# Performance work log

Hardware: AMD Instinct MI355X
Metric: run time of the kernel (lower is better)

## Reference

```python
import jax, jax.numpy as jnp
import numpy as np

BN_EPS = 1e-5

def _square_distance(src, dst):
    # src [B,N,3], dst [B,S,3] -> [B,N,S]
    d = -2.0 * jnp.einsum('bnc,bsc->bns', src, dst)
    d = d + jnp.sum(src * src, -1)[:, :, None]
    d = d + jnp.sum(dst * dst, -1)[:, None, :]
    return d

def _conv_bn_relu(x, w, b, g, beta):
    # x [B,C,N]; 1x1 conv == channel GEMM, then training-mode batchnorm over (B,N)
    y = jnp.einsum('oc,bcn->bon', w, x) + b[None, :, None]
    mean = jnp.mean(y, axis=(0, 2), keepdims=True)
    var = jnp.mean((y - mean) ** 2, axis=(0, 2), keepdims=True)  # biased, as torch BN uses for normalization
    y = (y - mean) * jax.lax.rsqrt(var + BN_EPS)
    y = y * g[None, :, None] + beta[None, :, None]
    return jax.nn.relu(y)

def setup_inputs() -> dict:
    key = jax.random.key(0)
    ks = jax.random.split(key, 8)
    B, N, S, D1, D2 = 8, 8192, 2048, 128, 256
    C_in, C_mid, C_out = D1 + D2, 256, 256
    return {
        'xyz1': jax.random.normal(ks[0], (B, 3, N), jnp.float32),
        'xyz2': jax.random.normal(ks[1], (B, 3, S), jnp.float32),
        'points1': jax.random.normal(ks[2], (B, D1, N), jnp.float32),
        'points2': jax.random.normal(ks[3], (B, D2, S), jnp.float32),
        'w1': jax.random.normal(ks[4], (C_mid, C_in), jnp.float32) * (1.0 / np.sqrt(C_in)),
        'b1': jax.random.normal(ks[5], (C_mid,), jnp.float32) * 0.01,
        'g1': jnp.ones((C_mid,), jnp.float32),
        'beta1': jnp.zeros((C_mid,), jnp.float32),
        'w2': jax.random.normal(ks[6], (C_out, C_mid), jnp.float32) * (1.0 / np.sqrt(C_mid)),
        'b2': jax.random.normal(ks[7], (C_out,), jnp.float32) * 0.01,
        'g2': jnp.ones((C_out,), jnp.float32),
        'beta2': jnp.zeros((C_out,), jnp.float32),
    }

def reference(xyz1, xyz2, points1, points2, w1, b1, g1, beta1, w2, b2, g2, beta2):
    B = xyz1.shape[0]
    p1xyz = jnp.transpose(xyz1, (0, 2, 1))      # [B,N,3]
    p2xyz = jnp.transpose(xyz2, (0, 2, 1))      # [B,S,3]
    p2 = jnp.transpose(points2, (0, 2, 1))      # [B,S,D2]

    dists = _square_distance(p1xyz, p2xyz)      # [B,N,S]
    neg_d3, idx = jax.lax.top_k(-dists, 3)      # 3 smallest distances
    d3 = -neg_d3                                # [B,N,3]
    recip = 1.0 / (d3 + 1e-8)
    weight = recip / jnp.sum(recip, axis=2, keepdims=True)  # [B,N,3]

    gathered = jax.vmap(lambda p, i: p[i])(p2, idx)          # [B,N,3,D2]
    interp = jnp.sum(gathered * weight[..., None], axis=2)   # [B,N,D2]

    new_points = jnp.concatenate([jnp.transpose(points1, (0, 2, 1)), interp], axis=-1)
    x = jnp.transpose(new_points, (0, 2, 1))    # [B,D1+D2,N]
    x = _conv_bn_relu(x, w1, b1, g1, beta1)
    x = _conv_bn_relu(x, w2, b2, g2, beta2)
    return x
```

## Files before the change

kernel.cpp:

```cpp
#include <hip/hip_runtime.h>

#define B_    8
#define N_    8192
#define S_    2048
#define D1_   128
#define D2_   256
#define CIN_  384
#define CMID_ 256
#define COUT_ 256

typedef unsigned int  u32;
typedef unsigned short u16;
typedef __attribute__((ext_vector_type(8))) short short8;
typedef __attribute__((ext_vector_type(4))) float f32x4;

static __device__ __forceinline__ u32 uminu(u32 a, u32 b) { return a < b ? a : b; }
static __device__ __forceinline__ u32 umaxu(u32 a, u32 b) { return a > b ? a : b; }
static __device__ __forceinline__ u32 umed3(u32 a, u32 b, u32 c) {
  u32 d;
  asm("v_med3_u32 %0, %1, %2, %3" : "=v"(d) : "v"(a), "v"(b), "v"(c));
  return d;
}
static __device__ __forceinline__ u16 f2bf(float f) {
  union { float f; u32 u; } v; v.f = f;
  u32 r = v.u + 0x7FFFu + ((v.u >> 16) & 1u);
  return (u16)(r >> 16);
}
static __device__ __forceinline__ float bflo(u32 u) { return __uint_as_float(u << 16); }
static __device__ __forceinline__ float bfhi(u32 u) { return __uint_as_float(u & 0xFFFF0000u); }

#define GLD16(g, l)                                                             \
  __builtin_amdgcn_global_load_lds((const __attribute__((address_space(1))) void*)(g), \
                                   (__attribute__((address_space(3))) void*)(l), 16, 0, 0)

__global__ __launch_bounds__(256) void k_prep(const float* __restrict__ xyz2,
                                              float4* __restrict__ pts4) {
  const int b = blockIdx.y, s = blockIdx.x * 256 + threadIdx.x;
  const float* xb = xyz2 + (size_t)b * 3 * S_;
  float x = xb[s], y = xb[S_ + s], z = xb[2 * S_ + s];
  pts4[b * S_ + s] = make_float4(-2.f * x, -2.f * y, -2.f * z, x * x + y * y + z * z);
}

__global__ __launch_bounds__(256) void k_nn_scan(const float* __restrict__ xyz1,
                                                 const float4* __restrict__ pts4,
                                                 uint4* __restrict__ keys) {
  const int b = blockIdx.z, chunk = blockIdx.y;
  const int n = blockIdx.x * 256 + threadIdx.x;
  const float* pb = xyz1 + (size_t)b * 3 * N_;
  const float px = pb[n], py = pb[N_ + n], pz = pb[2 * N_ + n];
  const float pn = px * px + py * py + pz * pz;
  const float4* __restrict__ P = pts4 + b * S_ + chunk * 256;
  u32 m0 = ~0u, m1 = ~0u, m2 = ~0u, m3 = ~0u;
#pragma unroll 8
  for (int s = 0; s < 256; ++s) {
    float4 q = P[s];
    float d = fmaf(px, q.x, fmaf(py, q.y, fmaf(pz, q.z, pn + q.w)));
    d = fmaxf(d, 0.f);
    u32 k = (__float_as_uint(d) & 0xFFFFFF00u) | (u32)s;
    m3 = uminu(m3, umaxu(m2, k));
    m2 = umed3(m1, m2, k);
    m1 = umed3(m0, m1, k);
    m0 = uminu(m0, k);
  }
  uint4 v; v.x = m0; v.y = m1; v.z = m2; v.w = m3;
  keys[((size_t)(b * 8 + chunk)) * N_ + n] = v;
}

__global__ __launch_bounds__(256) void k_refine(const float* __restrict__ xyz1,
                                                const float4* __restrict__ pts4,
                                                const uint4* __restrict__ keys,
                                                int4* __restrict__ idx4,
                                                float4* __restrict__ w4) {
  const int b = blockIdx.y, n = blockIdx.x * 256 + threadIdx.x;
  const float* pb = xyz1 + (size_t)b * 3 * N_;
  const double px = (double)pb[n], py = (double)pb[N_ + n], pz = (double)pb[2 * N_ + n];
  const double pn = px * px + py * py + pz * pz;
  double bd0 = 1e300, bd1 = 1e300, bd2 = 1e300;
  int bi0 = 1 << 30, bi1 = 1 << 30, bi2 = 1 << 30;
#pragma unroll
  for (int c = 0; c < 8; ++c) {
    uint4 kk = keys[((size_t)(b * 8 + c)) * N_ + n];
    u32 arr[4] = {kk.x, kk.y, kk.z, kk.w};
#pragma unroll
    for (int j = 0; j < 4; ++j) {
      int s = c * 256 + (int)(arr[j] & 255u);
      float4 q = pts4[b * S_ + s];
      double x = (double)(q.x * -0.5f), y = (double)(q.y * -0.5f), z = (double)(q.z * -0.5f);
      double dot = px * x + py * y + pz * z;
      double d = -2.0 * dot + (pn + (x * x + y * y + z * z));
      if (d < bd2 || (d == bd2 && s < bi2)) {
        if (d < bd1 || (d == bd1 && s < bi1)) {
          bd2 = bd1; bi2 = bi1;
          if (d < bd0 || (d == bd0 && s < bi0)) { bd1 = bd0; bi1 = bi0; bd0 = d; bi0 = s; }
          else                                  { bd1 = d;  bi1 = s; }
        } else { bd2 = d; bi2 = s; }
      }
    }
  }
  float f0 = (float)bd0, f1 = (float)bd1, f2 = (float)bd2;
  float r0 = 1.f / (f0 + 1e-8f), r1 = 1.f / (f1 + 1e-8f), r2 = 1.f / (f2 + 1e-8f);
  float rs = r0 + r1 + r2;
  w4[(size_t)b * N_ + n]   = make_float4(r0 / rs, r1 / rs, r2 / rs, 0.f);
  idx4[(size_t)b * N_ + n] = make_int4(bi0, bi1, bi2, 0);
}

__global__ __launch_bounds__(256) void k_p2t(const float* __restrict__ p2,
                                             float* __restrict__ p2T) {
  __shared__ float t[32][33];
  const int b = blockIdx.z, s0 = blockIdx.x * 32, d0 = blockIdx.y * 32;
  const int cc = threadIdx.x & 31, rr = threadIdx.x >> 5;
#pragma unroll
  for (int i = 0; i < 4; ++i) {
    int r = rr + i * 8;
    t[r][cc] = p2[((size_t)b * D2_ + d0 + r) * S_ + s0 + cc];
  }
  __syncthreads();
#pragma unroll
  for (int i = 0; i < 4; ++i) {
    int r = rr + i * 8;
    p2T[((size_t)b * S_ + s0 + r) * D2_ + d0 + cc] = t[cc][r];
  }
}

__global__ __launch_bounds__(256) void k_packp1(const float* __restrict__ p1,
                                                u16* __restrict__ xT) {
  __shared__ float t[32][33];
  const int b = blockIdx.z, n0 = blockIdx.x * 32, c0 = blockIdx.y * 32;
  const int cc = threadIdx.x & 31, rr = threadIdx.x >> 5;
#pragma unroll
  for (int i = 0; i < 4; ++i) {
    int r = rr + i * 8;
    t[r][cc] = p1[((size_t)b * D1_ + c0 + r) * N_ + n0 + cc];
  }
  __syncthreads();
#pragma unroll
  for (int i = 0; i < 4; ++i) {
    int r = rr + i * 8;
    xT[((size_t)b * N_ + n0 + r) * CIN_ + c0 + cc] = f2bf(t[cc][r]);
  }
}

__global__ __launch_bounds__(256) void k_gather_pack(const float* __restrict__ p2T,
                                                     const int4* __restrict__ idx4,
                                                     const float4* __restrict__ w4,
                                                     u16* __restrict__ xT) {
  const int b = blockIdx.y;
  const int wv = threadIdx.x >> 6, lane = threadIdx.x & 63;
  const int nbase = blockIdx.x * 16 + wv * 4;
  int4   id[4];
  float4 w[4];
#pragma unroll
  for (int i = 0; i < 4; ++i) {
    id[i] = idx4[(size_t)b * N_ + nbase + i];
    w[i]  = w4[(size_t)b * N_ + nbase + i];
  }
#pragma unroll
  for (int i = 0; i < 4; ++i) {
    const int n = nbase + i;
    const float4* r0 = (const float4*)(p2T + ((size_t)b * S_ + id[i].x) * D2_) + lane;
    const float4* r1 = (const float4*)(p2T + ((size_t)b * S_ + id[i].y) * D2_) + lane;
    const float4* r2 = (const float4*)(p2T + ((size_t)b * S_ + id[i].z) * D2_) + lane;
    float4 a = *r0, bb = *r1, cq = *r2;
    ushort4 pk;
    pk.x = f2bf(a.x * w[i].x + bb.x * w[i].y + cq.x * w[i].z);
    pk.y = f2bf(a.y * w[i].x + bb.y * w[i].y + cq.y * w[i].z);
    pk.z = f2bf(a.z * w[i].x + bb.z * w[i].y + cq.z * w[i].z);
    pk.w = f2bf(a.w * w[i].x + bb.w * w[i].y + cq.w * w[i].z);
    *(ushort4*)(xT + ((size_t)b * N_ + n) * CIN_ + D1_ + lane * 4) = pk;
  }
}

__global__ __launch_bounds__(256) void k_wcvt(const float* __restrict__ w1,
                                              const float* __restrict__ w2,
                                              u16* __restrict__ w1b,
                                              u16* __restrict__ w2b) {
  int i = blockIdx.x * 256 + threadIdx.x;
  if (i < CMID_ * CIN_) w1b[i] = f2bf(w1[i]);
  int j = i - CMID_ * CIN_;
  if (j >= 0 && j < COUT_ * CMID_) w2b[j] = f2bf(w2[j]);
}

__global__ __launch_bounds__(256) void k_gemm1(const u16* __restrict__ Wb,
                                               const float* __restrict__ bias,
                                               const u16* __restrict__ xT,
                                               u16* __restrict__ y1T,
                                               float* __restrict__ sum,
                                               float* __restrict__ sumsq) {
  __shared__ u16 As[2][4096];
  __shared__ u16 Bs[2][4096];
  __shared__ float s_sum[128], s_ssq[128];
  const int b = blockIdx.z, bm0 = blockIdx.y * 128, bn0 = blockIdx.x * 128;
  const int tid = threadIdx.x, w = tid >> 6, l = tid & 63;
  const int wm = w & 1, wn = w >> 1;
  const int lr = l >> 2, lc = l & 3;
  const int fm = l & 15, fq = l >> 4;
  const int clog = (lc ^ ((lr >> 1) & 3)) * 8;
  const int swz8 = (fq ^ ((fm >> 1) & 3)) * 8;
  if (tid < 128) { s_sum[tid] = 0.f; s_ssq[tid] = 0.f; }
  f32x4 acc[4][4];
#pragma unroll
  for (int i = 0; i < 4; ++i)
#pragma unroll
    for (int j = 0; j < 4; ++j) acc[i][j] = (f32x4){0.f, 0.f, 0.f, 0.f};

  const int NK = CIN_ / 32;
#pragma unroll
  for (int j = 0; j < 2; ++j) {
    int seg = w * 2 + j, row = seg * 16 + lr;
    GLD16(Wb + (size_t)(bm0 + row) * CIN_ + clog, &As[0][seg * 512]);
    GLD16(xT + ((size_t)b * N_ + bn0 + row) * CIN_ + clog, &Bs[0][seg * 512]);
  }
  for (int kk = 0; kk < NK; ++kk) {
    __syncthreads();
    const int cur = kk & 1;
    if (kk + 1 < NK) {
      const int k0 = (kk + 1) * 32, nxt = cur ^ 1;
#pragma unroll
      for (int j = 0; j < 2; ++j) {
        int seg = w * 2 + j, row = seg * 16 + lr;
        GLD16(Wb + (size_t)(bm0 + row) * CIN_ + k0 + clog, &As[nxt][seg * 512]);
        GLD16(xT + ((size_t)b * N_ + bn0 + row) * CIN_ + k0 + clog, &Bs[nxt][seg * 512]);
      }
    }
    short8 af[4], bfr[4];
#pragma unroll
    for (int f = 0; f < 4; ++f) {
      af[f]  = *(const short8*)&As[cur][(wm * 64 + f * 16 + fm) * 32 + swz8];
      bfr[f] = *(const short8*)&Bs[cur][(wn * 64 + f * 16 + fm) * 32 + swz8];
    }
#pragma unroll
    for (int i = 0; i < 4; ++i)
#pragma unroll
      for (int j = 0; j < 4; ++j)
        acc[i][j] = __builtin_amdgcn_mfma_f32_16x16x32_bf16(af[i], bfr[j], acc[i][j], 0, 0, 0);
  }
#pragma unroll
  for (int i = 0; i < 4; ++i) {
    int ob = bm0 + wm * 64 + i * 16 + fq * 4;
    float4 b4 = *(const float4*)(bias + ob);
    float sv0 = 0, sv1 = 0, sv2 = 0, sv3 = 0, qv0 = 0, qv1 = 0, qv2 = 0, qv3 = 0;
#pragma unroll
    for (int j = 0; j < 4; ++j) {
      int n = bn0 + wn * 64 + j * 16 + fm;
      ushort4 pk;
      pk.x = f2bf(acc[i][j][0] + b4.x);
      pk.y = f2bf(acc[i][j][1] + b4.y);
      pk.z = f2bf(acc[i][j][2] + b4.z);
      pk.w = f2bf(acc[i][j][3] + b4.w);
      *(ushort4*)(y1T + ((size_t)b * N_ + n) * CMID_ + ob) = pk;
      float v0 = bflo(pk.x), v1 = bflo(pk.y), v2 = bflo(pk.z), v3 = bflo(pk.w);
      sv0 += v0; sv1 += v1; sv2 += v2; sv3 += v3;
      qv0 = fmaf(v0, v0, qv0); qv1 = fmaf(v1, v1, qv1);
      qv2 = fmaf(v2, v2, qv2); qv3 = fmaf(v3, v3, qv3);
    }
#pragma unroll
    for (int m = 1; m <= 8; m <<= 1) {
      sv0 += __shfl_xor(sv0, m); sv1 += __shfl_xor(sv1, m);
      sv2 += __shfl_xor(sv2, m); sv3 += __shfl_xor(sv3, m);
      qv0 += __shfl_xor(qv0, m); qv1 += __shfl_xor(qv1, m);
      qv2 += __shfl_xor(qv2, m); qv3 += __shfl_xor(qv3, m);
    }
    if (fm == 0) {
      int ol = wm * 64 + i * 16 + fq * 4;
      atomicAdd(&s_sum[ol + 0], sv0); atomicAdd(&s_sum[ol + 1], sv1);
      atomicAdd(&s_sum[ol + 2], sv2); atomicAdd(&s_sum[ol + 3], sv3);
      atomicAdd(&s_ssq[ol + 0], qv0); atomicAdd(&s_ssq[ol + 1], qv1);
      atomicAdd(&s_ssq[ol + 2], qv2); atomicAdd(&s_ssq[ol + 3], qv3);
    }
  }
  __syncthreads();
  if (tid < 128) {
    atomicAdd(&sum[bm0 + tid], s_sum[tid]);
    atomicAdd(&sumsq[bm0 + tid], s_ssq[tid]);
  }
}

__global__ __launch_bounds__(256) void k_affine(const float* __restrict__ sum,
                                                const float* __restrict__ sumsq,
                                                const float* __restrict__ g,
                                                const float* __restrict__ beta,
                                                float* __restrict__ scale,
                                                float* __restrict__ shift) {
  int o = threadIdx.x;
  const float inv = 1.0f / (float)(B_ * N_);
  float m = sum[o] * inv;
  float var = sumsq[o] * inv - m * m;
  float sc = g[o] / sqrtf(var + 1e-5f);
  scale[o] = sc;
  shift[o] = beta[o] - m * sc;
}

__global__ __launch_bounds__(256) void k_gemm2(const u16* __restrict__ Wb2,
                                               const float* __restrict__ b2,
                                               const u16* __restrict__ y1T,
                                               const float* __restrict__ scale,
                                               const float* __restrict__ shift,
                                               u16* __restrict__ y2T,
                                               float* __restrict__ sum,
                                               float* __restrict__ sumsq) {
  __shared__ u16 As[2][4096];
  __shared__ u16 Bs[2][4096];
  __shared__ float s_sum[128], s_ssq[128];
  const int b = blockIdx.z, bm0 = blockIdx.y * 128, bn0 = blockIdx.x * 128;
  const int tid = threadIdx.x, w = tid >> 6, l = tid & 63;
  const int wm = w & 1, wn = w >> 1;
  const int lr = l >> 2, lc = l & 3;
  const int fm = l & 15, fq = l >> 4;
  const int clog = (lc ^ ((lr >> 1) & 3)) * 8;
  const int swz8 = (fq ^ ((fm >> 1) & 3)) * 8;
  const int bn_0 = tid >> 2, bcp0 = tid & 3;
  const int bn_1 = (tid + 256) >> 2, bcp1 = (tid + 256) & 3;
  const int bph0 = (bcp0 ^ ((bn_0 >> 1) & 3)) * 8;
  const int bph1 = (bcp1 ^ ((bn_1 >> 1) & 3)) * 8;
  if (tid < 128) { s_sum[tid] = 0.f; s_ssq[tid] = 0.f; }
  f32x4 acc[4][4];
#pragma unroll
  for (int i = 0; i < 4; ++i)
#pragma unroll
    for (int j = 0; j < 4; ++j) acc[i][j] = (f32x4){0.f, 0.f, 0.f, 0.f};

  const int NK = CMID_ / 32;

  auto bn_pack = [&](uint4 r, int c) -> uint4 {
    float4 sA = *(const float4*)(scale + c);
    float4 sB = *(const float4*)(scale + c + 4);
    float4 hA = *(const float4*)(shift + c);
    float4 hB = *(const float4*)(shift + c + 4);
    float v0 = fmaxf(fmaf(bflo(r.x), sA.x, hA.x), 0.f);
    float v1 = fmaxf(fmaf(bfhi(r.x), sA.y, hA.y), 0.f);
    float v2 = fmaxf(fmaf(bflo(r.y), sA.z, hA.z), 0.f);
    float v3 = fmaxf(fmaf(bfhi(r.y), sA.w, hA.w), 0.f);
    float v4 = fmaxf(fmaf(bflo(r.z), sB.x, hB.x), 0.f);
    float v5 = fmaxf(fmaf(bfhi(r.z), sB.y, hB.y), 0.f);
    float v6 = fmaxf(fmaf(bflo(r.w), sB.z, hB.z), 0.f);
    float v7 = fmaxf(fmaf(bfhi(r.w), sB.w, hB.w), 0.f);
    uint4 pk;
    pk.x = (u32)f2bf(v0) | ((u32)f2bf(v1) << 16);
    pk.y = (u32)f2bf(v2) | ((u32)f2bf(v3) << 16);
    pk.z = (u32)f2bf(v4) | ((u32)f2bf(v5) << 16);
    pk.w = (u32)f2bf(v6) | ((u32)f2bf(v7) << 16);
    return pk;
  };

  {
#pragma unroll
    for (int j = 0; j < 2; ++j) {
      int seg = w * 2 + j, row = seg * 16 + lr;
      GLD16(Wb2 + (size_t)(bm0 + row) * CMID_ + clog, &As[0][seg * 512]);
    }
    uint4 r0 = *(const uint4*)(y1T + ((size_t)b * N_ + bn0 + bn_0) * CMID_ + bcp0 * 8);
    uint4 r1 = *(const uint4*)(y1T + ((size_t)b * N_ + bn0 + bn_1) * CMID_ + bcp1 * 8);
    *(uint4*)&Bs[0][bn_0 * 32 + bph0] = bn_pack(r0, bcp0 * 8);
    *(uint4*)&Bs[0][bn_1 * 32 + bph1] = bn_pack(r1, bcp1 * 8);
  }
  for (int kk = 0; kk < NK; ++kk) {
    __syncthreads();
    const int cur = kk & 1;
    uint4 r0, r1;
    const bool have = (kk + 1 < NK);
    const int k0n = (kk + 1) * 32, nxt = cur ^ 1;
    if (have) {
      r0 = *(const uint4*)(y1T + ((size_t)b * N_ + bn0 + bn_0) * CMID_ + k0n + bcp0 * 8);
      r1 = *(const uint4*)(y1T + ((size_t)b * N_ + bn0 + bn_1) * CMID_ + k0n + bcp1 * 8);
#pragma unroll
      for (int j = 0; j < 2; ++j) {
        int seg = w * 2 + j, row = seg * 16 + lr;
        GLD16(Wb2 + (size_t)(bm0 + row) * CMID_ + k0n + clog, &As[nxt][seg * 512]);
      }
    }
    short8 af[4], bfr[4];
#pragma unroll
    for (int f = 0; f < 4; ++f) {
      af[f]  = *(const short8*)&As[cur][(wm * 64 + f * 16 + fm) * 32 + swz8];
      bfr[f] = *(const short8*)&Bs[cur][(wn * 64 + f * 16 + fm) * 32 + swz8];
    }
#pragma unroll
    for (int i = 0; i < 4; ++i)
#pragma unroll
      for (int j = 0; j < 4; ++j)
        acc[i][j] = __builtin_amdgcn_mfma_f32_16x16x32_bf16(af[i], bfr[j], acc[i][j], 0, 0, 0);
    if (have) {
      *(uint4*)&Bs[nxt][bn_0 * 32 + bph0] = bn_pack(r0, k0n + bcp0 * 8);
      *(uint4*)&Bs[nxt][bn_1 * 32 + bph1] = bn_pack(r1, k0n + bcp1 * 8);
    }
  }
#pragma unroll
  for (int i = 0; i < 4; ++i) {
    int ob = bm0 + wm * 64 + i * 16 + fq * 4;
    float4 b4 = *(const float4*)(b2 + ob);
    float sv0 = 0, sv1 = 0, sv2 = 0, sv3 = 0, qv0 = 0, qv1 = 0, qv2 = 0, qv3 = 0;
#pragma unroll
    for (int j = 0; j < 4; ++j) {
      int n = bn0 + wn * 64 + j * 16 + fm;
      ushort4 pk;
      pk.x = f2bf(acc[i][j][0] + b4.x);
      pk.y = f2bf(acc[i][j][1] + b4.y);
      pk.z = f2bf(acc[i][j][2] + b4.z);
      pk.w = f2bf(acc[i][j][3] + b4.w);
      *(ushort4*)(y2T + ((size_t)b * N_ + n) * COUT_ + ob) = pk;
      float v0 = bflo(pk.x), v1 = bflo(pk.y), v2 = bflo(pk.z), v3 = bflo(pk.w);
      sv0 += v0; sv1 += v1; sv2 += v2; sv3 += v3;
      qv0 = fmaf(v0, v0, qv0); qv1 = fmaf(v1, v1, qv1);
      qv2 = fmaf(v2, v2, qv2); qv3 = fmaf(v3, v3, qv3);
    }
#pragma unroll
    for (int m = 1; m <= 8; m <<= 1) {
      sv0 += __shfl_xor(sv0, m); sv1 += __shfl_xor(sv1, m);
      sv2 += __shfl_xor(sv2, m); sv3 += __shfl_xor(sv3, m);
      qv0 += __shfl_xor(qv0, m); qv1 += __shfl_xor(qv1, m);
      qv2 += __shfl_xor(qv2, m); qv3 += __shfl_xor(qv3, m);
    }
    if (fm == 0) {
      int ol = wm * 64 + i * 16 + fq * 4;
      atomicAdd(&s_sum[ol + 0], sv0); atomicAdd(&s_sum[ol + 1], sv1);
      atomicAdd(&s_sum[ol + 2], sv2); atomicAdd(&s_sum[ol + 3], sv3);
      atomicAdd(&s_ssq[ol + 0], qv0); atomicAdd(&s_ssq[ol + 1], qv1);
      atomicAdd(&s_ssq[ol + 2], qv2); atomicAdd(&s_ssq[ol + 3], qv3);
    }
  }
  __syncthreads();
  if (tid < 128) {
    atomicAdd(&sum[bm0 + tid], s_sum[tid]);
    atomicAdd(&sumsq[bm0 + tid], s_ssq[tid]);
  }
}

__global__ __launch_bounds__(256) void k_bn2t(const u16* __restrict__ y2T,
                                              const float* __restrict__ scale,
                                              const float* __restrict__ shift,
                                              float* __restrict__ out) {
  __shared__ float t[32][33];
  const int b = blockIdx.z, n0 = blockIdx.x * 32, o0 = blockIdx.y * 32;
  const int cc = threadIdx.x & 31, rr = threadIdx.x >> 5;
  const float sc = scale[o0 + cc], sh = shift[o0 + cc];
#pragma unroll
  for (int i = 0; i < 4; ++i) {
    int r = rr + i * 8;
    float v = bflo((u32)y2T[((size_t)b * N_ + n0 + r) * COUT_ + o0 + cc]);
    t[r][cc] = fmaxf(fmaf(v, sc, sh), 0.f);
  }
  __syncthreads();
#pragma unroll
  for (int i = 0; i < 4; ++i) {
    int r = rr + i * 8;
    out[((size_t)b * COUT_ + o0 + r) * N_ + n0 + cc] = t[cc][r];
  }
}

extern "C" void kernel_launch(void* const* d_in, const int* in_sizes, int n_in,
                              void* d_out, int out_size, void* d_ws, size_t ws_size,
                              hipStream_t stream) {
  const float* xyz1    = (const float*)d_in[0];
  const float* xyz2    = (const float*)d_in[1];
  const float* points1 = (const float*)d_in[2];
  const float* points2 = (const float*)d_in[3];
  const float* w1      = (const float*)d_in[4];
  const float* b1      = (const float*)d_in[5];
  const float* g1      = (const float*)d_in[6];
  const float* beta1   = (const float*)d_in[7];
  const float* w2      = (const float*)d_in[8];
  const float* b2      = (const float*)d_in[9];
  const float* g2      = (const float*)d_in[10];
  const float* beta2   = (const float*)d_in[11];
  float* out = (float*)d_out;

  char* ws = (char*)d_ws;
  size_t off = 0;
  u16*    xT    = (u16*)(ws + off);    off += (size_t)B_ * N_ * CIN_ * 2;
  u16*    y1T   = (u16*)(ws + off);    off += (size_t)B_ * N_ * CMID_ * 2;
  float*  p2T   = (float*)(ws + off);  off += (size_t)B_ * S_ * D2_ * 4;
  float4* pts4  = (float4*)(ws + off); off += (size_t)B_ * S_ * 16;
  uint4*  keys  = (uint4*)(ws + off);  off += (size_t)B_ * 8 * N_ * 16;
  int4*   idx4  = (int4*)(ws + off);   off += (size_t)B_ * N_ * 16;
  float4* w4    = (float4*)(ws + off); off += (size_t)B_ * N_ * 16;
  u16*    w1b   = (u16*)(ws + off);    off += (size_t)CMID_ * CIN_ * 2;
  u16*    w2b   = (u16*)(ws + off);    off += (size_t)COUT_ * CMID_ * 2;
  float*  stats = (float*)(ws + off);
  u16*    y2T   = xT;

  hipMemsetAsync(stats, 0, 1024 * sizeof(float), stream);

  k_wcvt       <<<dim3((CMID_ * CIN_ + COUT_ * CMID_) / 256), 256, 0, stream>>>(w1, w2, w1b, w2b);
  k_prep       <<<dim3(S_ / 256, B_), 256, 0, stream>>>(xyz2, pts4);
  k_p2t        <<<dim3(S_ / 32, D2_ / 32, B_), 256, 0, stream>>>(points2, p2T);
  k_nn_scan    <<<dim3(N_ / 256, 8, B_), 256, 0, stream>>>(xyz1, pts4, keys);
  k_refine     <<<dim3(N_ / 256, B_), 256, 0, stream>>>(xyz1, pts4, keys, idx4, w4);
  k_packp1     <<<dim3(N_ / 32, D1_ / 32, B_), 256, 0, stream>>>(points1, xT);
  k_gather_pack<<<dim3(N_ / 16, B_), 256, 0, stream>>>(p2T, idx4, w4, xT);
  k_gemm1      <<<dim3(N_ / 128, CMID_ / 128, B_), 256, 0, stream>>>(w1b, b1, xT, y1T,
                                                                     stats + 0, stats + 256);
  k_affine     <<<1, 256, 0, stream>>>(stats + 0, stats + 256, g1, beta1, stats + 1024, stats + 1280);
  k_gemm2      <<<dim3(N_ / 128, COUT_ / 128, B_), 256, 0, stream>>>(w2b, b2, y1T,
                                                                     stats + 1024, stats + 1280,
                                                                     y2T, stats + 512, stats + 768);
  k_affine     <<<1, 256, 0, stream>>>(stats + 512, stats + 768, g2, beta2, stats + 1536, stats + 1792);
  k_bn2t       <<<dim3(N_ / 32, COUT_ / 32, B_), 256, 0, stream>>>(y2T, stats + 1536, stats + 1792, out);
}
```

Measured before the change: 297.7 us.

## Load GEMM fragments directly from global into registers, drop LDS staging

```diff
diff --git a/kernel.cpp b/kernel.cpp
--- a/kernel.cpp
+++ b/kernel.cpp
@@ -28,10 +28,11 @@
 }
 static __device__ __forceinline__ float bflo(u32 u) { return __uint_as_float(u << 16); }
 static __device__ __forceinline__ float bfhi(u32 u) { return __uint_as_float(u & 0xFFFF0000u); }
-
-#define GLD16(g, l)                                                             \
-  __builtin_amdgcn_global_load_lds((const __attribute__((address_space(1))) void*)(g), \
-                                   (__attribute__((address_space(3))) void*)(l), 16, 0, 0)
+static __device__ __forceinline__ u32 cvtpk_bf16(float lo, float hi) {
+  u32 d;
+  asm("v_cvt_pk_bf16_f32 %0, %1, %2" : "=v"(d) : "v"(lo), "v"(hi));
+  return d;
+}
 
 __global__ __launch_bounds__(256) void k_prep(const float* __restrict__ xyz2,
                                               float4* __restrict__ pts4) {
@@ -180,60 +181,59 @@
   if (j >= 0 && j < COUT_ * CMID_) w2b[j] = f2bf(w2[j]);
 }
 
+#define MFMA16(AF, BF)                                                          \
+  {                                                                             \
+    _Pragma("unroll") for (int i_ = 0; i_ < 4; ++i_) {                          \
+      _Pragma("unroll") for (int j_ = 0; j_ < 4; ++j_) {                        \
+        acc[i_][j_] = __builtin_amdgcn_mfma_f32_16x16x32_bf16(                  \
+            AF[i_], BF[j_], acc[i_][j_], 0, 0, 0);                              \
+      }                                                                         \
+    }                                                                           \
+  }
+
 __global__ __launch_bounds__(256) void k_gemm1(const u16* __restrict__ Wb,
                                                const float* __restrict__ bias,
                                                const u16* __restrict__ xT,
                                                u16* __restrict__ y1T,
                                                float* __restrict__ sum,
                                                float* __restrict__ sumsq) {
-  __shared__ u16 As[2][4096];
-  __shared__ u16 Bs[2][4096];
   __shared__ float s_sum[128], s_ssq[128];
   const int b = blockIdx.z, bm0 = blockIdx.y * 128, bn0 = blockIdx.x * 128;
   const int tid = threadIdx.x, w = tid >> 6, l = tid & 63;
   const int wm = w & 1, wn = w >> 1;
-  const int lr = l >> 2, lc = l & 3;
   const int fm = l & 15, fq = l >> 4;
-  const int clog = (lc ^ ((lr >> 1) & 3)) * 8;
-  const int swz8 = (fq ^ ((fm >> 1) & 3)) * 8;
   if (tid < 128) { s_sum[tid] = 0.f; s_ssq[tid] = 0.f; }
+
+  const u16* Ab = Wb + (size_t)(bm0 + wm * 64 + fm) * CIN_ + fq * 8;
+  const u16* Bb = xT + ((size_t)b * N_ + bn0 + wn * 64 + fm) * CIN_ + fq * 8;
+
   f32x4 acc[4][4];
 #pragma unroll
   for (int i = 0; i < 4; ++i)
 #pragma unroll
     for (int j = 0; j < 4; ++j) acc[i][j] = (f32x4){0.f, 0.f, 0.f, 0.f};
 
+#define LDA_G1(dst, kk)                                                         \
+  { _Pragma("unroll") for (int i_ = 0; i_ < 4; ++i_)                            \
+      dst[i_] = *(const short8*)(Ab + (size_t)i_ * 16 * CIN_ + (kk) * 32); }
+#define LDB_G1(dst, kk)                                                         \
+  { _Pragma("unroll") for (int i_ = 0; i_ < 4; ++i_)                            \
+      dst[i_] = *(const short8*)(Bb + (size_t)i_ * 16 * CIN_ + (kk) * 32); }
+
   const int NK = CIN_ / 32;
-#pragma unroll
-  for (int j = 0; j < 2; ++j) {
-    int seg = w * 2 + j, row = seg * 16 + lr;
-    GLD16(Wb + (size_t)(bm0 + row) * CIN_ + clog, &As[0][seg * 512]);
-    GLD16(xT + ((size_t)b * N_ + bn0 + row) * CIN_ + clog, &Bs[0][seg * 512]);
-  }
-  for (int kk = 0; kk < NK; ++kk) {
-    __syncthreads();
-    const int cur = kk & 1;
-    if (kk + 1 < NK) {
-      const int k0 = (kk + 1) * 32, nxt = cur ^ 1;
-#pragma unroll
-      for (int j = 0; j < 2; ++j) {
-        int seg = w * 2 + j, row = seg * 16 + lr;
-        GLD16(Wb + (size_t)(bm0 + row) * CIN_ + k0 + clog, &As[nxt][seg * 512]);
-        GLD16(xT + ((size_t)b * N_ + bn0 + row) * CIN_ + k0 + clog, &Bs[nxt][seg * 512]);
-      }
-    }
-    short8 af[4], bfr[4];
-#pragma unroll
-    for (int f = 0; f < 4; ++f) {
-      af[f]  = *(const short8*)&As[cur][(wm * 64 + f * 16 + fm) * 32 + swz8];
-      bfr[f] = *(const short8*)&Bs[cur][(wn * 64 + f * 16 + fm) * 32 + swz8];
-    }
-#pragma unroll
-    for (int i = 0; i < 4; ++i)
-#pragma unroll
-      for (int j = 0; j < 4; ++j)
-        acc[i][j] = __builtin_amdgcn_mfma_f32_16x16x32_bf16(af[i], bfr[j], acc[i][j], 0, 0, 0);
-  }
+  short8 A0[4], B0[4], A1[4], B1[4];
+  LDA_G1(A0, 0); LDB_G1(B0, 0);
+#pragma unroll
+  for (int kk = 0; kk < NK; kk += 2) {
+    if (kk + 1 < NK) { LDA_G1(A1, kk + 1); LDB_G1(B1, kk + 1); }
+    MFMA16(A0, B0);
+    if (kk + 2 < NK) { LDA_G1(A0, kk + 2); LDB_G1(B0, kk + 2); }
+    if (kk + 1 < NK) MFMA16(A1, B1);
+  }
+#undef LDA_G1
+#undef LDB_G1
+
+  __syncthreads();
 #pragma unroll
   for (int i = 0; i < 4; ++i) {
     int ob = bm0 + wm * 64 + i * 16 + fq * 4;
@@ -298,92 +298,74 @@
                                                u16* __restrict__ y2T,
                                                float* __restrict__ sum,
                                                float* __restrict__ sumsq) {
-  __shared__ u16 As[2][4096];
-  __shared__ u16 Bs[2][4096];
   __shared__ float s_sum[128], s_ssq[128];
+  __shared__ float s_sc[CMID_], s_sh[CMID_];
   const int b = blockIdx.z, bm0 = blockIdx.y * 128, bn0 = blockIdx.x * 128;
   const int tid = threadIdx.x, w = tid >> 6, l = tid & 63;
   const int wm = w & 1, wn = w >> 1;
-  const int lr = l >> 2, lc = l & 3;
   const int fm = l & 15, fq = l >> 4;
-  const int clog = (lc ^ ((lr >> 1) & 3)) * 8;
-  const int swz8 = (fq ^ ((fm >> 1) & 3)) * 8;
-  const int bn_0 = tid >> 2, bcp0 = tid & 3;
-  const int bn_1 = (tid + 256) >> 2, bcp1 = (tid + 256) & 3;
-  const int bph0 = (bcp0 ^ ((bn_0 >> 1) & 3)) * 8;
-  const int bph1 = (bcp1 ^ ((bn_1 >> 1) & 3)) * 8;
   if (tid < 128) { s_sum[tid] = 0.f; s_ssq[tid] = 0.f; }
+  s_sc[tid] = scale[tid];
+  s_sh[tid] = shift[tid];
+  __syncthreads();
+
+  const u16* Ab = Wb2 + (size_t)(bm0 + wm * 64 + fm) * CMID_ + fq * 8;
+  const u16* Bb = y1T + ((size_t)b * N_ + bn0 + wn * 64 + fm) * CMID_ + fq * 8;
+
   f32x4 acc[4][4];
 #pragma unroll
   for (int i = 0; i < 4; ++i)
 #pragma unroll
     for (int j = 0; j < 4; ++j) acc[i][j] = (f32x4){0.f, 0.f, 0.f, 0.f};
 
+#define LDA_G2(dst, kk)                                                         \
+  { _Pragma("unroll") for (int i_ = 0; i_ < 4; ++i_)                            \
+      dst[i_] = *(const short8*)(Ab + (size_t)i_ * 16 * CMID_ + (kk) * 32); }
+#define LDR_G2(dst, kk)                                                         \
+  { _Pragma("unroll") for (int i_ = 0; i_ < 4; ++i_)                            \
+      dst[i_] = *(const uint4*)(Bb + (size_t)i_ * 16 * CMID_ + (kk) * 32); }
+#define BNCVT(BF, RF, kk)                                                       \
+  {                                                                             \
+    float4 s0_ = *(const float4*)&s_sc[(kk) * 32 + fq * 8];                     \
+    float4 s1_ = *(const float4*)&s_sc[(kk) * 32 + fq * 8 + 4];                 \
+    float4 h0_ = *(const float4*)&s_sh[(kk) * 32 + fq * 8];                     \
+    float4 h1_ = *(const float4*)&s_sh[(kk) * 32 + fq * 8 + 4];                 \
+    _Pragma("unroll") for (int j_ = 0; j_ < 4; ++j_) {                          \
+      uint4 r_ = RF[j_];                                                        \
+      float v0_ = fmaxf(fmaf(bflo(r_.x), s0_.x, h0_.x), 0.f);                   \
+      float v1_ = fmaxf(fmaf(bfhi(r_.x), s0_.y, h0_.y), 0.f);                   \
+      float v2_ = fmaxf(fmaf(bflo(r_.y), s0_.z, h0_.z), 0.f);                   \
+      float v3_ = fmaxf(fmaf(bfhi(r_.y), s0_.w, h0_.w), 0.f);                   \
+      float v4_ = fmaxf(fmaf(bflo(r_.z), s1_.x, h1_.x), 0.f);                   \
+      float v5_ = fmaxf(fmaf(bfhi(r_.z), s1_.y, h1_.y), 0.f);                   \
+      float v6_ = fmaxf(fmaf(bflo(r_.w), s1_.z, h1_.z), 0.f);                   \
+      float v7_ = fmaxf(fmaf(bfhi(r_.w), s1_.w, h1_.w), 0.f);                   \
+      union { u32 u[4]; short8 s; } cv_;                                        \
+      cv_.u[0] = cvtpk_bf16(v0_, v1_); cv_.u[1] = cvtpk_bf16(v2_, v3_);         \
+      cv_.u[2] = cvtpk_bf16(v4_, v5_); cv_.u[3] = cvtpk_bf16(v6_, v7_);         \
+      BF[j_] = cv_.s;                                                           \
+    }                                                                           \
+  }
+
   const int NK = CMID_ / 32;
-
-  auto bn_pack = [&](uint4 r, int c) -> uint4 {
-    float4 sA = *(const float4*)(scale + c);
-    float4 sB = *(const float4*)(scale + c + 4);
-    float4 hA = *(const float4*)(shift + c);
-    float4 hB = *(const float4*)(shift + c + 4);
-    float v0 = fmaxf(fmaf(bflo(r.x), sA.x, hA.x), 0.f);
-    float v1 = fmaxf(fmaf(bfhi(r.x), sA.y, hA.y), 0.f);
-    float v2 = fmaxf(fmaf(bflo(r.y), sA.z, hA.z), 0.f);
-    float v3 = fmaxf(fmaf(bfhi(r.y), sA.w, hA.w), 0.f);
-    float v4 = fmaxf(fmaf(bflo(r.z), sB.x, hB.x), 0.f);
-    float v5 = fmaxf(fmaf(bfhi(r.z), sB.y, hB.y), 0.f);
-    float v6 = fmaxf(fmaf(bflo(r.w), sB.z, hB.z), 0.f);
-    float v7 = fmaxf(fmaf(bfhi(r.w), sB.w, hB.w), 0.f);
-    uint4 pk;
-    pk.x = (u32)f2bf(v0) | ((u32)f2bf(v1) << 16);
-    pk.y = (u32)f2bf(v2) | ((u32)f2bf(v3) << 16);
-    pk.z = (u32)f2bf(v4) | ((u32)f2bf(v5) << 16);
-    pk.w = (u32)f2bf(v6) | ((u32)f2bf(v7) << 16);
-    return pk;
-  };
-
-  {
-#pragma unroll
-    for (int j = 0; j < 2; ++j) {
-      int seg = w * 2 + j, row = seg * 16 + lr;
-      GLD16(Wb2 + (size_t)(bm0 + row) * CMID_ + clog, &As[0][seg * 512]);
-    }
-    uint4 r0 = *(const uint4*)(y1T + ((size_t)b * N_ + bn0 + bn_0) * CMID_ + bcp0 * 8);
-    uint4 r1 = *(const uint4*)(y1T + ((size_t)b * N_ + bn0 + bn_1) * CMID_ + bcp1 * 8);
-    *(uint4*)&Bs[0][bn_0 * 32 + bph0] = bn_pack(r0, bcp0 * 8);
-    *(uint4*)&Bs[0][bn_1 * 32 + bph1] = bn_pack(r1, bcp1 * 8);
-  }
-  for (int kk = 0; kk < NK; ++kk) {
-    __syncthreads();
-    const int cur = kk & 1;
-    uint4 r0, r1;
-    const bool have = (kk + 1 < NK);
-    const int k0n = (kk + 1) * 32, nxt = cur ^ 1;
-    if (have) {
-      r0 = *(const uint4*)(y1T + ((size_t)b * N_ + bn0 + bn_0) * CMID_ + k0n + bcp0 * 8);
-      r1 = *(const uint4*)(y1T + ((size_t)b * N_ + bn0 + bn_1) * CMID_ + k0n + bcp1 * 8);
-#pragma unroll
-      for (int j = 0; j < 2; ++j) {
-        int seg = w * 2 + j, row = seg * 16 + lr;
-        GLD16(Wb2 + (size_t)(bm0 + row) * CMID_ + k0n + clog, &As[nxt][seg * 512]);
-      }
-    }
-    short8 af[4], bfr[4];
-#pragma unroll
-    for (int f = 0; f < 4; ++f) {
-      af[f]  = *(const short8*)&As[cur][(wm * 64 + f * 16 + fm) * 32 + swz8];
-      bfr[f] = *(const short8*)&Bs[cur][(wn * 64 + f * 16 + fm) * 32 + swz8];
-    }
-#pragma unroll
-    for (int i = 0; i < 4; ++i)
-#pragma unroll
-      for (int j = 0; j < 4; ++j)
-        acc[i][j] = __builtin_amdgcn_mfma_f32_16x16x32_bf16(af[i], bfr[j], acc[i][j], 0, 0, 0);
-    if (have) {
-      *(uint4*)&Bs[nxt][bn_0 * 32 + bph0] = bn_pack(r0, k0n + bcp0 * 8);
-      *(uint4*)&Bs[nxt][bn_1 * 32 + bph1] = bn_pack(r1, k0n + bcp1 * 8);
-    }
-  }
+  short8 A0[4], A1[4], Bf[4];
+  uint4  R0[4], R1[4];
+  LDA_G2(A0, 0); LDR_G2(R0, 0);
+#pragma unroll
+  for (int kk = 0; kk < NK; kk += 2) {
+    if (kk + 1 < NK) { LDA_G2(A1, kk + 1); LDR_G2(R1, kk + 1); }
+    BNCVT(Bf, R0, kk);
+    MFMA16(A0, Bf);
+    if (kk + 2 < NK) { LDA_G2(A0, kk + 2); LDR_G2(R0, kk + 2); }
+    if (kk + 1 < NK) {
+      BNCVT(Bf, R1, kk + 1);
+      MFMA16(A1, Bf);
+    }
+  }
+#undef LDA_G2
+#undef LDR_G2
+#undef BNCVT
+
 #pragma unroll
   for (int i = 0; i < 4; ++i) {
     int ob = bm0 + wm * 64 + i * 16 + fq * 4;
```

New measurement: 333.7 us. +12.1%, slower.

## Tile intermediate activations for direct LDS loads and replace BN atomics with partials

Applied to the files above, without the earlier changes.

```diff
diff --git a/kernel.cpp b/kernel.cpp
--- a/kernel.cpp
+++ b/kernel.cpp
@@ -28,6 +28,11 @@
 }
 static __device__ __forceinline__ float bflo(u32 u) { return __uint_as_float(u << 16); }
 static __device__ __forceinline__ float bfhi(u32 u) { return __uint_as_float(u & 0xFFFF0000u); }
+static __device__ __forceinline__ u32 cvtpk_bf16(float lo, float hi) {
+  u32 d;
+  asm("v_cvt_pk_bf16_f32 %0, %1, %2" : "=v"(d) : "v"(lo), "v"(hi));
+  return d;
+}
 
 #define GLD16(g, l)                                                             \
   __builtin_amdgcn_global_load_lds((const __attribute__((address_space(1))) void*)(g), \
@@ -180,12 +185,37 @@
   if (j >= 0 && j < COUT_ * CMID_) w2b[j] = f2bf(w2[j]);
 }
 
+__global__ __launch_bounds__(64) void k_bnstat(const float* __restrict__ ps,
+                                               const float* __restrict__ pq,
+                                               const float* __restrict__ g,
+                                               const float* __restrict__ beta,
+                                               float* __restrict__ scale,
+                                               float* __restrict__ shift) {
+  const int o = blockIdx.x, l = threadIdx.x;
+  float s = 0.f, q = 0.f;
+#pragma unroll
+  for (int i = 0; i < 8; ++i) {
+    s += ps[(size_t)o * 512 + i * 64 + l];
+    q += pq[(size_t)o * 512 + i * 64 + l];
+  }
+#pragma unroll
+  for (int m = 1; m <= 32; m <<= 1) { s += __shfl_xor(s, m); q += __shfl_xor(q, m); }
+  if (l == 0) {
+    const float inv = 1.0f / (float)(B_ * N_);
+    float mean = s * inv;
+    float var = q * inv - mean * mean;
+    float sc = g[o] / sqrtf(var + 1e-5f);
+    scale[o] = sc;
+    shift[o] = beta[o] - mean * sc;
+  }
+}
+
 __global__ __launch_bounds__(256) void k_gemm1(const u16* __restrict__ Wb,
                                                const float* __restrict__ bias,
                                                const u16* __restrict__ xT,
                                                u16* __restrict__ y1T,
-                                               float* __restrict__ sum,
-                                               float* __restrict__ sumsq) {
+                                               float* __restrict__ psum,
+                                               float* __restrict__ pssq) {
   __shared__ u16 As[2][4096];
   __shared__ u16 Bs[2][4096];
   __shared__ float s_sum[128], s_ssq[128];
@@ -234,6 +264,7 @@
       for (int j = 0; j < 4; ++j)
         acc[i][j] = __builtin_amdgcn_mfma_f32_16x16x32_bf16(af[i], bfr[j], acc[i][j], 0, 0, 0);
   }
+  u16* tb = y1T + ((size_t)b * 64 + (bn0 >> 7)) * 32768;
 #pragma unroll
   for (int i = 0; i < 4; ++i) {
     int ob = bm0 + wm * 64 + i * 16 + fq * 4;
@@ -241,13 +272,13 @@
     float sv0 = 0, sv1 = 0, sv2 = 0, sv3 = 0, qv0 = 0, qv1 = 0, qv2 = 0, qv3 = 0;
 #pragma unroll
     for (int j = 0; j < 4; ++j) {
-      int n = bn0 + wn * 64 + j * 16 + fm;
+      int nl = wn * 64 + j * 16 + fm;
       ushort4 pk;
       pk.x = f2bf(acc[i][j][0] + b4.x);
       pk.y = f2bf(acc[i][j][1] + b4.y);
       pk.z = f2bf(acc[i][j][2] + b4.z);
       pk.w = f2bf(acc[i][j][3] + b4.w);
-      *(ushort4*)(y1T + ((size_t)b * N_ + n) * CMID_ + ob) = pk;
+      *(ushort4*)(tb + (size_t)(ob >> 5) * 4096 + nl * 32 + (ob & 31)) = pk;
       float v0 = bflo(pk.x), v1 = bflo(pk.y), v2 = bflo(pk.z), v3 = bflo(pk.w);
       sv0 += v0; sv1 += v1; sv2 += v2; sv3 += v3;
       qv0 = fmaf(v0, v0, qv0); qv1 = fmaf(v1, v1, qv1);
@@ -270,24 +301,10 @@
   }
   __syncthreads();
   if (tid < 128) {
-    atomicAdd(&sum[bm0 + tid], s_sum[tid]);
-    atomicAdd(&sumsq[bm0 + tid], s_ssq[tid]);
-  }
-}
-
-__global__ __launch_bounds__(256) void k_affine(const float* __restrict__ sum,
-                                                const float* __restrict__ sumsq,
-                                                const float* __restrict__ g,
-                                                const float* __restrict__ beta,
-                                                float* __restrict__ scale,
-                                                float* __restrict__ shift) {
-  int o = threadIdx.x;
-  const float inv = 1.0f / (float)(B_ * N_);
-  float m = sum[o] * inv;
-  float var = sumsq[o] * inv - m * m;
-  float sc = g[o] / sqrtf(var + 1e-5f);
-  scale[o] = sc;
-  shift[o] = beta[o] - m * sc;
+    const int blk = blockIdx.x + 64 * blockIdx.z;
+    psum[(size_t)(bm0 + tid) * 512 + blk] = s_sum[tid];
+    pssq[(size_t)(bm0 + tid) * 512 + blk] = s_ssq[tid];
+  }
 }
 
 __global__ __launch_bounds__(256) void k_gemm2(const u16* __restrict__ Wb2,
@@ -296,11 +313,12 @@
                                                const float* __restrict__ scale,
                                                const float* __restrict__ shift,
                                                u16* __restrict__ y2T,
-                                               float* __restrict__ sum,
-                                               float* __restrict__ sumsq) {
+                                               float* __restrict__ psum,
+                                               float* __restrict__ pssq) {
   __shared__ u16 As[2][4096];
   __shared__ u16 Bs[2][4096];
   __shared__ float s_sum[128], s_ssq[128];
+  __shared__ float s_sc[CMID_], s_sh[CMID_];
   const int b = blockIdx.z, bm0 = blockIdx.y * 128, bn0 = blockIdx.x * 128;
   const int tid = threadIdx.x, w = tid >> 6, l = tid & 63;
   const int wm = w & 1, wn = w >> 1;
@@ -308,82 +326,63 @@
   const int fm = l & 15, fq = l >> 4;
   const int clog = (lc ^ ((lr >> 1) & 3)) * 8;
   const int swz8 = (fq ^ ((fm >> 1) & 3)) * 8;
-  const int bn_0 = tid >> 2, bcp0 = tid & 3;
-  const int bn_1 = (tid + 256) >> 2, bcp1 = (tid + 256) & 3;
-  const int bph0 = (bcp0 ^ ((bn_0 >> 1) & 3)) * 8;
-  const int bph1 = (bcp1 ^ ((bn_1 >> 1) & 3)) * 8;
   if (tid < 128) { s_sum[tid] = 0.f; s_ssq[tid] = 0.f; }
+  s_sc[tid] = scale[tid];
+  s_sh[tid] = shift[tid];
   f32x4 acc[4][4];
 #pragma unroll
   for (int i = 0; i < 4; ++i)
 #pragma unroll
     for (int j = 0; j < 4; ++j) acc[i][j] = (f32x4){0.f, 0.f, 0.f, 0.f};
 
+  const u16* tb = y1T + ((size_t)b * 64 + (bn0 >> 7)) * 32768;
   const int NK = CMID_ / 32;
-
-  auto bn_pack = [&](uint4 r, int c) -> uint4 {
-    float4 sA = *(const float4*)(scale + c);
-    float4 sB = *(const float4*)(scale + c + 4);
-    float4 hA = *(const float4*)(shift + c);
-    float4 hB = *(const float4*)(shift + c + 4);
-    float v0 = fmaxf(fmaf(bflo(r.x), sA.x, hA.x), 0.f);
-    float v1 = fmaxf(fmaf(bfhi(r.x), sA.y, hA.y), 0.f);
-    float v2 = fmaxf(fmaf(bflo(r.y), sA.z, hA.z), 0.f);
-    float v3 = fmaxf(fmaf(bfhi(r.y), sA.w, hA.w), 0.f);
-    float v4 = fmaxf(fmaf(bflo(r.z), sB.x, hB.x), 0.f);
-    float v5 = fmaxf(fmaf(bfhi(r.z), sB.y, hB.y), 0.f);
-    float v6 = fmaxf(fmaf(bflo(r.w), sB.z, hB.z), 0.f);
-    float v7 = fmaxf(fmaf(bfhi(r.w), sB.w, hB.w), 0.f);
-    uint4 pk;
-    pk.x = (u32)f2bf(v0) | ((u32)f2bf(v1) << 16);
-    pk.y = (u32)f2bf(v2) | ((u32)f2bf(v3) << 16);
-    pk.z = (u32)f2bf(v4) | ((u32)f2bf(v5) << 16);
-    pk.w = (u32)f2bf(v6) | ((u32)f2bf(v7) << 16);
-    return pk;
-  };
-
-  {
-#pragma unroll
-    for (int j = 0; j < 2; ++j) {
-      int seg = w * 2 + j, row = seg * 16 + lr;
-      GLD16(Wb2 + (size_t)(bm0 + row) * CMID_ + clog, &As[0][seg * 512]);
-    }
-    uint4 r0 = *(const uint4*)(y1T + ((size_t)b * N_ + bn0 + bn_0) * CMID_ + bcp0 * 8);
-    uint4 r1 = *(const uint4*)(y1T + ((size_t)b * N_ + bn0 + bn_1) * CMID_ + bcp1 * 8);
-    *(uint4*)&Bs[0][bn_0 * 32 + bph0] = bn_pack(r0, bcp0 * 8);
-    *(uint4*)&Bs[0][bn_1 * 32 + bph1] = bn_pack(r1, bcp1 * 8);
+#pragma unroll
+  for (int j = 0; j < 2; ++j) {
+    int seg = w * 2 + j, row = seg * 16 + lr;
+    GLD16(Wb2 + (size_t)(bm0 + row) * CMID_ + clog, &As[0][seg * 512]);
+    GLD16(tb + row * 32 + clog, &Bs[0][seg * 512]);
   }
   for (int kk = 0; kk < NK; ++kk) {
     __syncthreads();
     const int cur = kk & 1;
-    uint4 r0, r1;
-    const bool have = (kk + 1 < NK);
-    const int k0n = (kk + 1) * 32, nxt = cur ^ 1;
-    if (have) {
-      r0 = *(const uint4*)(y1T + ((size_t)b * N_ + bn0 + bn_0) * CMID_ + k0n + bcp0 * 8);
-      r1 = *(const uint4*)(y1T + ((size_t)b * N_ + bn0 + bn_1) * CMID_ + k0n + bcp1 * 8);
+    if (kk + 1 < NK) {
+      const int nxt = cur ^ 1;
 #pragma unroll
       for (int j = 0; j < 2; ++j) {
         int seg = w * 2 + j, row = seg * 16 + lr;
-        GLD16(Wb2 + (size_t)(bm0 + row) * CMID_ + k0n + clog, &As[nxt][seg * 512]);
+        GLD16(Wb2 + (size_t)(bm0 + row) * CMID_ + (kk + 1) * 32 + clog, &As[nxt][seg * 512]);
+        GLD16(tb + (size_t)(kk + 1) * 4096 + row * 32 + clog, &Bs[nxt][seg * 512]);
       }
     }
+    const int kb = kk * 32 + fq * 8;
+    float4 s0 = *(const float4*)&s_sc[kb], s1 = *(const float4*)&s_sc[kb + 4];
+    float4 h0 = *(const float4*)&s_sh[kb], h1 = *(const float4*)&s_sh[kb + 4];
     short8 af[4], bfr[4];
 #pragma unroll
     for (int f = 0; f < 4; ++f) {
-      af[f]  = *(const short8*)&As[cur][(wm * 64 + f * 16 + fm) * 32 + swz8];
-      bfr[f] = *(const short8*)&Bs[cur][(wn * 64 + f * 16 + fm) * 32 + swz8];
+      af[f] = *(const short8*)&As[cur][(wm * 64 + f * 16 + fm) * 32 + swz8];
+      uint4 r = *(const uint4*)&Bs[cur][(wn * 64 + f * 16 + fm) * 32 + swz8];
+      float v0 = fmaxf(fmaf(bflo(r.x), s0.x, h0.x), 0.f);
+      float v1 = fmaxf(fmaf(bfhi(r.x), s0.y, h0.y), 0.f);
+      float v2 = fmaxf(fmaf(bflo(r.y), s0.z, h0.z), 0.f);
+      float v3 = fmaxf(fmaf(bfhi(r.y), s0.w, h0.w), 0.f);
+      float v4 = fmaxf(fmaf(bflo(r.z), s1.x, h1.x), 0.f);
+      float v5 = fmaxf(fmaf(bfhi(r.z), s1.y, h1.y), 0.f);
+      float v6 = fmaxf(fmaf(bflo(r.w), s1.z, h1.z), 0.f);
+      float v7 = fmaxf(fmaf(bfhi(r.w), s1.w, h1.w), 0.f);
+      union { u32 u[4]; short8 s; } cv;
+      cv.u[0] = cvtpk_bf16(v0, v1); cv.u[1] = cvtpk_bf16(v2, v3);
+      cv.u[2] = cvtpk_bf16(v4, v5); cv.u[3] = cvtpk_bf16(v6, v7);
+      bfr[f] = cv.s;
     }
 #pragma unroll
     for (int i = 0; i < 4; ++i)
 #pragma unroll
       for (int j = 0; j < 4; ++j)
         acc[i][j] = __builtin_amdgcn_mfma_f32_16x16x32_bf16(af[i], bfr[j], acc[i][j], 0, 0, 0);
-    if (have) {
-      *(uint4*)&Bs[nxt][bn_0 * 32 + bph0] = bn_pack(r0, k0n + bcp0 * 8);
-      *(uint4*)&Bs[nxt][bn_1 * 32 + bph1] = bn_pack(r1, k0n + bcp1 * 8);
-    }
-  }
+  }
+  u16* tb2 = y2T + ((size_t)b * 64 + (bn0 >> 7)) * 32768;
 #pragma unroll
   for (int i = 0; i < 4; ++i) {
     int ob = bm0 + wm * 64 + i * 16 + fq * 4;
@@ -391,13 +390,13 @@
     float sv0 = 0, sv1 = 0, sv2 = 0, sv3 = 0, qv0 = 0, qv1 = 0, qv2 = 0, qv3 = 0;
 #pragma unroll
     for (int j = 0; j < 4; ++j) {
-      int n = bn0 + wn * 64 + j * 16 + fm;
+      int nl = wn * 64 + j * 16 + fm;
       ushort4 pk;
       pk.x = f2bf(acc[i][j][0] + b4.x);
       pk.y = f2bf(acc[i][j][1] + b4.y);
       pk.z = f2bf(acc[i][j][2] + b4.z);
       pk.w = f2bf(acc[i][j][3] + b4.w);
-      *(ushort4*)(y2T + ((size_t)b * N_ + n) * COUT_ + ob) = pk;
+      *(ushort4*)(tb2 + (size_t)(ob >> 5) * 4096 + nl * 32 + (ob & 31)) = pk;
       float v0 = bflo(pk.x), v1 = bflo(pk.y), v2 = bflo(pk.z), v3 = bflo(pk.w);
       sv0 += v0; sv1 += v1; sv2 += v2; sv3 += v3;
       qv0 = fmaf(v0, v0, qv0); qv1 = fmaf(v1, v1, qv1);
@@ -420,8 +419,9 @@
   }
   __syncthreads();
   if (tid < 128) {
-    atomicAdd(&sum[bm0 + tid], s_sum[tid]);
-    atomicAdd(&sumsq[bm0 + tid], s_ssq[tid]);
+    const int blk = blockIdx.x + 64 * blockIdx.z;
+    psum[(size_t)(bm0 + tid) * 512 + blk] = s_sum[tid];
+    pssq[(size_t)(bm0 + tid) * 512 + blk] = s_ssq[tid];
   }
 }
 
@@ -433,10 +433,12 @@
   const int b = blockIdx.z, n0 = blockIdx.x * 32, o0 = blockIdx.y * 32;
   const int cc = threadIdx.x & 31, rr = threadIdx.x >> 5;
   const float sc = scale[o0 + cc], sh = shift[o0 + cc];
+  const u16* tb = y2T + ((size_t)b * 64 + (n0 >> 7)) * 32768 +
+                  (size_t)(o0 >> 5) * 4096 + (size_t)(n0 & 96) * 32;
 #pragma unroll
   for (int i = 0; i < 4; ++i) {
     int r = rr + i * 8;
-    float v = bflo((u32)y2T[((size_t)b * N_ + n0 + r) * COUT_ + o0 + cc]);
+    float v = bflo((u32)tb[r * 32 + cc]);
     t[r][cc] = fmaxf(fmaf(v, sc, sh), 0.f);
   }
   __syncthreads();
@@ -477,8 +479,12 @@
   u16*    w2b   = (u16*)(ws + off);    off += (size_t)COUT_ * CMID_ * 2;
   float*  stats = (float*)(ws + off);
   u16*    y2T   = xT;
-
-  hipMemsetAsync(stats, 0, 1024 * sizeof(float), stream);
+  float* psum1 = (float*)keys;
+  float* pssq1 = psum1 + 256 * 512;
+  float* psum2 = pssq1 + 256 * 512;
+  float* pssq2 = psum2 + 256 * 512;
+  float* scale1 = stats,        * shift1 = stats + 256;
+  float* scale2 = stats + 512,  * shift2 = stats + 768;
 
   k_wcvt       <<<dim3((CMID_ * CIN_ + COUT_ * CMID_) / 256), 256, 0, stream>>>(w1, w2, w1b, w2b);
   k_prep       <<<dim3(S_ / 256, B_), 256, 0, stream>>>(xyz2, pts4);
@@ -488,11 +494,11 @@
   k_packp1     <<<dim3(N_ / 32, D1_ / 32, B_), 256, 0, stream>>>(points1, xT);
   k_gather_pack<<<dim3(N_ / 16, B_), 256, 0, stream>>>(p2T, idx4, w4, xT);
   k_gemm1      <<<dim3(N_ / 128, CMID_ / 128, B_), 256, 0, stream>>>(w1b, b1, xT, y1T,
-                                                                     stats + 0, stats + 256);
-  k_affine     <<<1, 256, 0, stream>>>(stats + 0, stats + 256, g1, beta1, stats + 1024, stats + 1280);
+                                                                     psum1, pssq1);
+  k_bnstat     <<<dim3(CMID_), 64, 0, stream>>>(psum1, pssq1, g1, beta1, scale1, shift1);
   k_gemm2      <<<dim3(N_ / 128, COUT_ / 128, B_), 256, 0, stream>>>(w2b, b2, y1T,
-                                                                     stats + 1024, stats + 1280,
-                                                                     y2T, stats + 512, stats + 768);
-  k_affine     <<<1, 256, 0, stream>>>(stats + 512, stats + 768, g2, beta2, stats + 1536, stats + 1792);
-  k_bn2t       <<<dim3(N_ / 32, COUT_ / 32, B_), 256, 0, stream>>>(y2T, stats + 1536, stats + 1792, out);
-}
+                                                                     scale1, shift1,
+                                                                     y2T, psum2, pssq2);
+  k_bnstat     <<<dim3(COUT_), 64, 0, stream>>>(psum2, pssq2, g2, beta2, scale2, shift2);
+  k_bn2t       <<<dim3(N_ / 32, COUT_ / 32, B_), 256, 0, stream>>>(y2T, scale2, shift2, out);
+}
```

Measured after the change: 287.1 us. 3.6% less time.
